# Kernel optimization log

Hardware: AMD Instinct MI355X
Metric: run time of the kernel (lower is better)

The kernel has to match this reference:

```python
import jax, jax.numpy as jnp
import numpy as np

SCALING = 2.0  # lora scaling attached via set_lora (lora_alpha / r)


def setup_inputs() -> dict:
    key = jax.random.key(0)
    ks = jax.random.split(key, 8)
    E, DIN, DOUT, N, K, R = 8, 2048, 2048, 4096, 2, 16
    inputs = jax.random.normal(ks[0], (N, DIN), jnp.float32)
    weight = jax.random.normal(ks[1], (E, DOUT, DIN), jnp.float32) * 0.02
    lora_A = jax.random.normal(ks[2], (E, R, DIN), jnp.float32) * 0.02
    lora_B = jax.random.normal(ks[3], (E, DOUT, R), jnp.float32) * 0.02
    gates = jax.nn.softmax(jax.random.normal(ks[4], (N, K), jnp.float32), axis=-1)
    # expert assignment per (token, slot); scattermoe contract:
    #   sorted_scattered_idxs = argsort(assign); token = idx // k, slot = idx % k
    assign = jax.random.randint(ks[5], (N * K,), 0, E)
    sorted_scattered_idxs = jnp.argsort(assign).astype(jnp.int32)
    sorted_expert_idxs = assign[sorted_scattered_idxs].astype(jnp.int32)
    counts = jnp.bincount(assign, length=E)
    expert_offsets = jnp.cumsum(counts).astype(jnp.int32)
    return dict(inputs=inputs, weight=weight, lora_A=lora_A, lora_B=lora_B,
                gates=gates, sorted_expert_idxs=sorted_expert_idxs,
                sorted_scattered_idxs=sorted_scattered_idxs,
                expert_offsets=expert_offsets, k=K)


def reference(inputs, weight, lora_A, lora_B, gates, sorted_expert_idxs,
              sorted_scattered_idxs, expert_offsets, k):
    # Fused LoRA grouped GEMM:  Y = X @ W + scaling * (X @ A^T) @ B^T
    # grouped_in=False, grouped_out=False, bias=None (module defaults).
    E = weight.shape[0]
    N = gates.shape[0]
    W = jnp.swapaxes(weight, 1, 2)          # [E, din, dout] (weight.permute(0,2,1))
    token = sorted_scattered_idxs // k      # source token per sorted slot
    slot = sorted_scattered_idxs % k        # which of the k routes
    x = inputs[token]                       # gather -> [N*k, din]
    y = jnp.zeros((x.shape[0], W.shape[2]), x.dtype)
    for e in range(E):                      # fixed small expert loop
        m = (sorted_expert_idxs == e)[:, None]
        xe = jnp.where(m, x, 0.0)
        y = y + (xe @ W[e] + SCALING * ((xe @ jnp.swapaxes(lora_A[e], 0, 1)) @ jnp.swapaxes(lora_B[e], 0, 1)))
    g = gates[token, slot][:, None]         # gate per sorted slot
    out = jnp.zeros((N, W.shape[2]), y.dtype).at[token].add(y * g)
    return out
```

## Files before the change

kernel.cpp:

```cpp
#include <hip/hip_runtime.h>
#include <hip/hip_bf16.h>

#define E_    8
#define DIN   2048
#define DOUT  2048
#define N_TOK 4096
#define NK    8192
#define R_    16
#define KEXT  2112
#define KT_N  (KEXT / 64)

typedef __bf16 bf16x8 __attribute__((ext_vector_type(8)));
typedef float  f32x4  __attribute__((ext_vector_type(4)));
typedef unsigned short u16x8 __attribute__((ext_vector_type(8)));

static __device__ __forceinline__ void gld16(const void* g, void* l) {
  __builtin_amdgcn_global_load_lds(
      (const __attribute__((address_space(1))) unsigned int*)g,
      (__attribute__((address_space(3))) unsigned int*)l, 16, 0, 0);
}

static __device__ __forceinline__ float bfu2f(unsigned short u) {
  union { unsigned int u; float f; } v; v.u = ((unsigned int)u) << 16; return v.f;
}
static __device__ __forceinline__ unsigned short f2bfu(float f) {
  union { float f; unsigned int u; } v; v.f = f;
  unsigned int r = v.u + 0x7fffu + ((v.u >> 16) & 1u);
  return (unsigned short)(r >> 16);
}

__global__ void __launch_bounds__(64)
k_wconv(const float* __restrict__ w, const float* __restrict__ lb,
        unsigned short* __restrict__ wbe) {
  const long long row = blockIdx.x;
  const float4* src  = (const float4*)(w + row * DIN);
  const float4* lsrc = (const float4*)(lb + row * R_);
  ushort4* dst = (ushort4*)(wbe + row * KEXT);
  for (int u = threadIdx.x; u < KEXT / 4; u += 64) {
    float4 v;
    if (u < 512)       v = src[u];
    else if (u < 516)  v = lsrc[u - 512];
    else               v = make_float4(0.f, 0.f, 0.f, 0.f);
    ushort4 o;
    o.x = f2bfu(v.x); o.y = f2bfu(v.y); o.z = f2bfu(v.z); o.w = f2bfu(v.w);
    dst[u] = o;
  }
}

__global__ void k_aconv(const float* __restrict__ a, unsigned short* __restrict__ ab) {
  long long i = (long long)blockIdx.x * blockDim.x + threadIdx.x;
  float4 v = ((const float4*)a)[i];
  ushort4 o;
  o.x = f2bfu(v.x); o.y = f2bfu(v.y); o.z = f2bfu(v.z); o.w = f2bfu(v.w);
  ((ushort4*)ab)[i] = o;
}

__global__ void k_gather(const float* __restrict__ x, const int* __restrict__ ssi,
                         const float* __restrict__ gates, const int* __restrict__ kptr,
                         unsigned short* __restrict__ Xe, float* __restrict__ gate,
                         int* __restrict__ tok) {
  int s = blockIdx.x;
  int ssv = ssi[s];
  int kk = kptr[0];
  int t = ssv / kk, sl = ssv - t * kk;
  if (threadIdx.x == 0) { gate[s] = gates[t * kk + sl]; tok[s] = t; }
  const float4* src = (const float4*)(x + (long long)t * DIN);
  ushort4* dst = (ushort4*)(Xe + (long long)s * KEXT);
  for (int i = threadIdx.x; i < 512; i += 256) {
    float4 v = src[i];
    ushort4 o;
    o.x = f2bfu(v.x); o.y = f2bfu(v.y); o.z = f2bfu(v.z); o.w = f2bfu(v.w);
    dst[i] = o;
  }
  if (threadIdx.x < 12) {
    ushort4 z; z.x = z.y = z.z = z.w = 0;
    dst[516 + threadIdx.x] = z;
  }
}

__global__ void __launch_bounds__(64)
k_xa(unsigned short* __restrict__ Xe, const unsigned short* __restrict__ Ab,
     const int* __restrict__ sei) {
  const int s = blockIdx.x;
  const int tid = threadIdx.x;
  const int e = sei[s];
  const u16x8* xr = (const u16x8*)(Xe + (long long)s * KEXT);
  float xf[32];
#pragma unroll
  for (int i = 0; i < 4; i++) {
    u16x8 xv = xr[tid + i * 64];
#pragma unroll
    for (int t = 0; t < 8; t++) xf[i * 8 + t] = bfu2f(xv[t]);
  }
#pragma unroll
  for (int r = 0; r < 16; r++) {
    const u16x8* ar = (const u16x8*)(Ab + ((long long)e * R_ + r) * DIN);
    float acc = 0.f;
#pragma unroll
    for (int i = 0; i < 4; i++) {
      u16x8 av = ar[tid + i * 64];
#pragma unroll
      for (int t = 0; t < 8; t++) acc += xf[i * 8 + t] * bfu2f(av[t]);
    }
    acc += __shfl_xor(acc, 1);  acc += __shfl_xor(acc, 2);
    acc += __shfl_xor(acc, 4);  acc += __shfl_xor(acc, 8);
    acc += __shfl_xor(acc, 16); acc += __shfl_xor(acc, 32);
    if (tid == 0) Xe[(long long)s * KEXT + 2048 + r] = f2bfu(2.0f * acc);
  }
}

__global__ void __launch_bounds__(256)
k_gemm(const unsigned short* __restrict__ Xe, const unsigned short* __restrict__ Wbe,
       const float* __restrict__ gate, const int* __restrict__ tok,
       const int* __restrict__ eoff, float* __restrict__ out) {
  __shared__ alignas(16) unsigned short sAB[2 * 128 * 64];
  __shared__ float gs[128];
  __shared__ int   ts[128];

  int tile = blockIdx.x;
  int off_prev = 0, e = -1, m_start = 0, m_end = 0, acc_t = 0;
#pragma unroll
  for (int i = 0; i < E_; i++) {
    int oe = eoff[i];
    int Me = oe - off_prev;
    int te = (Me + 127) >> 7;
    if (e < 0 && tile < acc_t + te) {
      e = i; m_start = off_prev + (tile - acc_t) * 128; m_end = oe;
    }
    acc_t += te;
    off_prev = oe;
  }
  if (e < 0) return;
  const int n_start = blockIdx.y * 128;

  const int tid = threadIdx.x;
  const int w = tid >> 6, lane = tid & 63;
  const int wm = w & 1, wn = w >> 1;
  const int quad = lane >> 4, l15 = lane & 15;

  if (tid < 128) {
    int gm = m_start + tid; if (gm >= m_end) gm = m_end - 1;
    gs[tid] = gate[gm];
    ts[tid] = tok[gm];
  }

  f32x4 acc[4][4];
#pragma unroll
  for (int mi = 0; mi < 4; mi++)
#pragma unroll
    for (int ni = 0; ni < 4; ni++)
      acc[mi][ni] = (f32x4){0.f, 0.f, 0.f, 0.f};

  const int srow = lane >> 3;
  const int scol = ((lane & 7) ^ srow) * 8;
  const unsigned short* Wbase = Wbe + (long long)e * DOUT * KEXT;

  for (int kt = 0; kt < KT_N; kt++) {
    const int k0 = kt * 64;
#pragma unroll
    for (int j = 0; j < 4; j++) {
      int c = w * 4 + j;
      int rt = c * 8 + srow;
      int ga = m_start + rt; if (ga >= m_end) ga = m_end - 1;
      gld16(Xe + (long long)ga * KEXT + k0 + scol, &sAB[c * 512 + lane * 8]);
      gld16(Wbase + (long long)(n_start + rt) * KEXT + k0 + scol,
            &sAB[8192 + c * 512 + lane * 8]);
    }
    __syncthreads();
#pragma unroll
    for (int ks = 0; ks < 2; ks++) {
      const int kx = (((ks << 2) | quad) ^ (l15 & 7)) << 3;
      bf16x8 af[4], bfr[4];
#pragma unroll
      for (int mi = 0; mi < 4; mi++)
        af[mi] = *(const bf16x8*)&sAB[(wm * 64 + mi * 16 + l15) * 64 + kx];
#pragma unroll
      for (int ni = 0; ni < 4; ni++)
        bfr[ni] = *(const bf16x8*)&sAB[8192 + (wn * 64 + ni * 16 + l15) * 64 + kx];
#pragma unroll
      for (int mi = 0; mi < 4; mi++)
#pragma unroll
        for (int ni = 0; ni < 4; ni++)
          acc[mi][ni] = __builtin_amdgcn_mfma_f32_16x16x32_bf16(
              af[mi], bfr[ni], acc[mi][ni], 0, 0, 0);
    }
    __syncthreads();
  }

#pragma unroll
  for (int ni = 0; ni < 4; ni++) {
    int n = n_start + wn * 64 + ni * 16 + l15;
#pragma unroll
    for (int mi = 0; mi < 4; mi++) {
#pragma unroll
      for (int t4 = 0; t4 < 4; t4++) {
        int row = wm * 64 + mi * 16 + quad * 4 + t4;
        if (m_start + row >= m_end) continue;
        float o = acc[mi][ni][t4] * gs[row];
        atomicAdd(out + (long long)ts[row] * DOUT + n, o);
      }
    }
  }
}

extern "C" void kernel_launch(void* const* d_in, const int* in_sizes, int n_in,
                              void* d_out, int out_size, void* d_ws, size_t ws_size,
                              hipStream_t stream) {
  (void)in_sizes; (void)n_in; (void)out_size; (void)ws_size;
  const float* inputs = (const float*)d_in[0];
  const float* weight = (const float*)d_in[1];
  const float* lora_A = (const float*)d_in[2];
  const float* lora_B = (const float*)d_in[3];
  const float* gates  = (const float*)d_in[4];
  const int* sei  = (const int*)d_in[5];
  const int* ssi  = (const int*)d_in[6];
  const int* eoff = (const int*)d_in[7];
  const int* kptr = (const int*)d_in[8];
  float* out = (float*)d_out;

  unsigned char* ws = (unsigned char*)d_ws;
  unsigned short* Wbe = (unsigned short*)ws;
  unsigned short* Xe  = (unsigned short*)(ws + 69206016);
  unsigned short* Ab  = (unsigned short*)(ws + 103809024);
  float* gate = (float*)(ws + 104333312);
  int*   tok  = (int*)(ws + 104366080);

  hipMemsetAsync(d_out, 0, (size_t)N_TOK * DOUT * sizeof(float), stream);
  k_wconv<<<E_ * DOUT, 64, 0, stream>>>(weight, lora_B, Wbe);
  k_aconv<<<256, 256, 0, stream>>>(lora_A, Ab);
  k_gather<<<NK, 256, 0, stream>>>(inputs, ssi, gates, kptr, Xe, gate, tok);
  k_xa<<<NK, 64, 0, stream>>>(Xe, Ab, sei);
  dim3 g(72, 16);
  k_gemm<<<g, 256, 0, stream>>>(Xe, Wbe, gate, tok, eoff, out);
}
```

Baseline: 446.3 us.

## Compute LoRA XA with per-expert MFMA tiles and remap GEMM grid by XCD

The per-row scalar dot-product kernel for X@A^T is replaced by an MFMA kernel that covers 16-row tiles per expert, using expert offsets instead of per-slot expert ids. This cuts the number of blocks and reuses A rows across 16 tokens, though each lane still loads straight from global memory. The main GEMM now runs on a flattened 1D grid whose block index is remapped so that each XCD gets two N-columns of tiles across all M tiles. The aim is better L2 reuse of weight tiles within each XCD.

Measured after the change: 435.2 us. 2.5% less time.

```diff
diff --git a/kernel.cpp b/kernel.cpp
--- a/kernel.cpp
+++ b/kernel.cpp
@@ -20,9 +20,6 @@
       (__attribute__((address_space(3))) unsigned int*)l, 16, 0, 0);
 }
 
-static __device__ __forceinline__ float bfu2f(unsigned short u) {
-  union { unsigned int u; float f; } v; v.u = ((unsigned int)u) << 16; return v.f;
-}
 static __device__ __forceinline__ unsigned short f2bfu(float f) {
   union { float f; unsigned int u; } v; v.f = f;
   unsigned int r = v.u + 0x7fffu + ((v.u >> 16) & 1u);
@@ -80,32 +77,36 @@
 
 __global__ void __launch_bounds__(64)
 k_xa(unsigned short* __restrict__ Xe, const unsigned short* __restrict__ Ab,
-     const int* __restrict__ sei) {
-  const int s = blockIdx.x;
-  const int tid = threadIdx.x;
-  const int e = sei[s];
-  const u16x8* xr = (const u16x8*)(Xe + (long long)s * KEXT);
-  float xf[32];
-#pragma unroll
-  for (int i = 0; i < 4; i++) {
-    u16x8 xv = xr[tid + i * 64];
-#pragma unroll
-    for (int t = 0; t < 8; t++) xf[i * 8 + t] = bfu2f(xv[t]);
-  }
-#pragma unroll
-  for (int r = 0; r < 16; r++) {
-    const u16x8* ar = (const u16x8*)(Ab + ((long long)e * R_ + r) * DIN);
-    float acc = 0.f;
-#pragma unroll
-    for (int i = 0; i < 4; i++) {
-      u16x8 av = ar[tid + i * 64];
-#pragma unroll
-      for (int t = 0; t < 8; t++) acc += xf[i * 8 + t] * bfu2f(av[t]);
-    }
-    acc += __shfl_xor(acc, 1);  acc += __shfl_xor(acc, 2);
-    acc += __shfl_xor(acc, 4);  acc += __shfl_xor(acc, 8);
-    acc += __shfl_xor(acc, 16); acc += __shfl_xor(acc, 32);
-    if (tid == 0) Xe[(long long)s * KEXT + 2048 + r] = f2bfu(2.0f * acc);
+     const int* __restrict__ eoff) {
+  int tile = blockIdx.x;
+  int off_prev = 0, e = -1, m_start = 0, m_end = 0, acc_t = 0;
+#pragma unroll
+  for (int i = 0; i < E_; i++) {
+    int oe = eoff[i];
+    int te = (oe - off_prev + 15) >> 4;
+    if (e < 0 && tile < acc_t + te) {
+      e = i; m_start = off_prev + (tile - acc_t) * 16; m_end = oe;
+    }
+    acc_t += te; off_prev = oe;
+  }
+  if (e < 0) return;
+  const int lane = threadIdx.x;
+  const int l15 = lane & 15, quad = lane >> 4;
+  int arow = m_start + l15; if (arow >= m_end) arow = m_end - 1;
+  const unsigned short* xp = Xe + (long long)arow * KEXT + quad * 8;
+  const unsigned short* bp = Ab + ((long long)e * R_ + l15) * DIN + quad * 8;
+  f32x4 acc = (f32x4){0.f, 0.f, 0.f, 0.f};
+#pragma unroll 8
+  for (int k0 = 0; k0 < DIN; k0 += 32) {
+    bf16x8 a = *(const bf16x8*)(xp + k0);
+    bf16x8 b = *(const bf16x8*)(bp + k0);
+    acc = __builtin_amdgcn_mfma_f32_16x16x32_bf16(a, b, acc, 0, 0, 0);
+  }
+#pragma unroll
+  for (int t = 0; t < 4; t++) {
+    int slot = m_start + quad * 4 + t;
+    if (slot < m_end)
+      Xe[(long long)slot * KEXT + 2048 + l15] = f2bfu(2.0f * acc[t]);
   }
 }
 
@@ -117,21 +118,24 @@
   __shared__ float gs[128];
   __shared__ int   ts[128];
 
-  int tile = blockIdx.x;
+  const int id = blockIdx.x;
+  const int xcd = id & 7, local = id >> 3;
+  const int mt = local % 72;
+  const int nt = (xcd << 1) | (local / 72);
+  const int n_start = nt << 7;
+
   int off_prev = 0, e = -1, m_start = 0, m_end = 0, acc_t = 0;
 #pragma unroll
   for (int i = 0; i < E_; i++) {
     int oe = eoff[i];
-    int Me = oe - off_prev;
-    int te = (Me + 127) >> 7;
-    if (e < 0 && tile < acc_t + te) {
-      e = i; m_start = off_prev + (tile - acc_t) * 128; m_end = oe;
+    int te = (oe - off_prev + 127) >> 7;
+    if (e < 0 && mt < acc_t + te) {
+      e = i; m_start = off_prev + (mt - acc_t) * 128; m_end = oe;
     }
     acc_t += te;
     off_prev = oe;
   }
   if (e < 0) return;
-  const int n_start = blockIdx.y * 128;
 
   const int tid = threadIdx.x;
   const int w = tid >> 6, lane = tid & 63;
@@ -216,6 +220,7 @@
   const int* ssi  = (const int*)d_in[6];
   const int* eoff = (const int*)d_in[7];
   const int* kptr = (const int*)d_in[8];
+  (void)sei;
   float* out = (float*)d_out;
 
   unsigned char* ws = (unsigned char*)d_ws;
@@ -229,7 +234,6 @@
   k_wconv<<<E_ * DOUT, 64, 0, stream>>>(weight, lora_B, Wbe);
   k_aconv<<<256, 256, 0, stream>>>(lora_A, Ab);
   k_gather<<<NK, 256, 0, stream>>>(inputs, ssi, gates, kptr, Xe, gate, tok);
-  k_xa<<<NK, 64, 0, stream>>>(Xe, Ab, sei);
-  dim3 g(72, 16);
-  k_gemm<<<g, 256, 0, stream>>>(Xe, Wbe, gate, tok, eoff, out);
-}
+  k_xa<<<519, 64, 0, stream>>>(Xe, Ab, eoff);
+  k_gemm<<<1152, 256, 0, stream>>>(Xe, Wbe, gate, tok, eoff, out);
+}
```
